# Kernel tuning notes

Measured on AMD Instinct MI355X. Metric: run time of the kernel, lower is better.

Reference implementation:

```python
import jax, jax.numpy as jnp
import numpy as np

H = 8      # heads
D = 64     # dim_head
DIM = 512  # model dim (== H*D)
LN_EPS = 1e-5


def setup_inputs() -> dict:
    key = jax.random.key(0)
    ks = jax.random.split(key, 4)
    B, N = 8, 1024
    x = jax.random.normal(ks[0], (B, N, DIM), dtype=jnp.float32)
    # params (torch Linear y = x @ W^T; we store W already transposed as (in, out))
    w_qkv = jax.random.normal(ks[1], (DIM, 3 * H * D), dtype=jnp.float32) * (DIM ** -0.5)
    w_out = jax.random.normal(ks[2], (H * D, DIM), dtype=jnp.float32) * ((H * D) ** -0.5)
    b_out = jnp.zeros((DIM,), dtype=jnp.float32)
    ln_g = jnp.ones((DIM,), dtype=jnp.float32)
    ln_b = jnp.zeros((DIM,), dtype=jnp.float32)
    return {"x": x, "w_qkv": w_qkv, "w_out": w_out, "b_out": b_out,
            "ln_g": ln_g, "ln_b": ln_b}


def reference(x, w_qkv, w_out, b_out, ln_g, ln_b):
    b, n, _ = x.shape
    qkv = x @ w_qkv                                   # [b, n, 3*H*D]
    q, k, v = jnp.split(qkv, 3, axis=-1)              # each [b, n, H*D]

    def to_heads(t):                                  # 'b n (h d) -> (b h) n d'
        return t.reshape(b, n, H, D).transpose(0, 2, 1, 3).reshape(b * H, n, D)

    q = to_heads(q)
    k = to_heads(k)
    v = to_heads(v)

    # FAITHFUL to source: k.view(b*h, -1, n) is a row-major reshape, NOT a
    # transpose, and NO scale is applied (self.scale is unused in forward).
    k_r = k.reshape(b * H, D, n)                      # [(bh), D, n] reinterpreted
    dots = jnp.matmul(q, k_r)                          # [(bh), n, n]
    attn = jax.nn.softmax(dots, axis=-1)
    out = jnp.matmul(attn, v)                          # [(bh), n, D]

    # '(b h) n d -> b n (h d)'
    out = out.reshape(b, H, n, D).transpose(0, 2, 1, 3).reshape(b, n, H * D)
    out = out @ w_out + b_out                          # to_out Linear (dropout=0)

    mu = jnp.mean(out, axis=-1, keepdims=True)
    var = jnp.var(out, axis=-1, keepdims=True)
    out = (out - mu) * jax.lax.rsqrt(var + LN_EPS) * ln_g + ln_b
    return out + x
```

## Files before the change

### kernel.cpp

```cpp
#include <hip/hip_runtime.h>

typedef unsigned short u16;
typedef unsigned int u32;
typedef __attribute__((ext_vector_type(4))) float f32x4;
typedef __attribute__((ext_vector_type(8))) short s16x8;

__device__ __forceinline__ u16 bf16_rne(float f) {
    u32 u = __float_as_uint(f);
    u32 r = u + 0x7FFFu + ((u >> 16) & 1u);
    return (u16)(r >> 16);
}

__device__ __forceinline__ u32 cvt_pk_bf16(float lo, float hi) {
    u32 r;
    asm("v_cvt_pk_bf16_f32 %0, %1, %2" : "=v"(r) : "v"(lo), "v"(hi));
    return r;
}

__device__ __forceinline__ void gl_lds16(const void* g, void* l) {
    __builtin_amdgcn_global_load_lds(
        (const __attribute__((address_space(1))) u32*)g,
        (__attribute__((address_space(3))) u32*)l, 16, 0, 0);
}

#define MFMA16(a, b, c) __builtin_amdgcn_mfma_f32_16x16x32_bf16((a), (b), (c), 0, 0, 0)

__global__ __launch_bounds__(256) void k_convert(const float* __restrict__ in,
                                                 u16* __restrict__ out, int n4) {
    int i = blockIdx.x * 256 + threadIdx.x;
    if (i >= n4) return;
    f32x4 v = *(const f32x4*)(in + (size_t)i * 4);
    u32 lo = cvt_pk_bf16(v.x, v.y);
    u32 hi = cvt_pk_bf16(v.z, v.w);
    u32* p = (u32*)(out + (size_t)i * 4);
    p[0] = lo;
    p[1] = hi;
}

__global__ __launch_bounds__(256) void k_transpose2(const float* __restrict__ w_qkv,
                                                    const float* __restrict__ w_out,
                                                    u16* __restrict__ wqkvt,
                                                    u16* __restrict__ woutt) {
    __shared__ float tile[32][33];
    const float* in;
    u16* out;
    int C, bxc;
    if (blockIdx.x < 48) { in = w_qkv; out = wqkvt; C = 1536; bxc = blockIdx.x; }
    else                 { in = w_out; out = woutt; C = 512;  bxc = blockIdx.x - 48; }
    const int R = 512;
    int bx = bxc * 32;
    int by = blockIdx.y * 32;
    int tx = threadIdx.x;
    int ty = threadIdx.y;
#pragma unroll
    for (int i = 0; i < 32; i += 8)
        tile[ty + i][tx] = in[(size_t)(by + ty + i) * C + bx + tx];
    __syncthreads();
#pragma unroll
    for (int i = 0; i < 32; i += 8)
        out[(size_t)(bx + ty + i) * R + by + tx] = bf16_rne(tile[tx][ty + i]);
}

__global__ __launch_bounds__(256) void k_qkv_gemm(
    const u16* __restrict__ xbf, const u16* __restrict__ wt,
    u16* __restrict__ qh, u16* __restrict__ kRT, u16* __restrict__ vT) {
    __shared__ __align__(16) u16 lA[2][128 * 64];
    __shared__ __align__(16) u16 lB[2][128 * 64];
    const int tid = threadIdx.x;
    const int lane = tid & 63, l15 = lane & 15, l4 = lane >> 4;
    const int wid = tid >> 6, wm = wid >> 1, wn = wid & 1;
    const int hw = blockIdx.x;
    const int e = hw & 7, idx = hw >> 3;
    const int m0 = (e + 8 * (idx / 12)) * 128;
    const int c0 = (idx % 12) * 128;

    const char* gA = (const char*)xbf + (size_t)m0 * 1024;
    const char* gB = (const char*)wt + (size_t)c0 * 1024;
    const int srow = tid >> 3;
    const int scol = (tid & 7) * 16;

    const f32x4 z4 = {0.f, 0.f, 0.f, 0.f};
    f32x4 acc[4][4];
#pragma unroll
    for (int i = 0; i < 4; ++i)
#pragma unroll
        for (int j = 0; j < 4; ++j) acc[i][j] = z4;

    auto stage = [&](int buf, int kt) {
#pragma unroll
        for (int q = 0; q < 4; ++q) {
            int row = q * 32 + srow;
            int sc = scol ^ ((row & 7) << 4);
            gl_lds16(gA + (size_t)row * 1024 + kt * 128 + sc,
                     (char*)lA[buf] + q * 4096 + tid * 16);
            gl_lds16(gB + (size_t)row * 1024 + kt * 128 + sc,
                     (char*)lB[buf] + q * 4096 + tid * 16);
        }
    };

    stage(0, 0);
    __syncthreads();
    for (int kt = 0; kt < 8; ++kt) {
        int buf = kt & 1;
        if (kt < 7) stage(buf ^ 1, kt + 1);
        s16x8 af[4][2], bfr[4][2];
#pragma unroll
        for (int i = 0; i < 4; ++i)
#pragma unroll
            for (int k2 = 0; k2 < 2; ++k2) {
                int ra = wm * 64 + i * 16 + l15;
                int ca = (k2 * 64 + l4 * 16) ^ ((ra & 7) << 4);
                af[i][k2] = *(const s16x8*)((const char*)lA[buf] + ra * 128 + ca);
                int rb = wn * 64 + i * 16 + l15;
                int cb = (k2 * 64 + l4 * 16) ^ ((rb & 7) << 4);
                bfr[i][k2] = *(const s16x8*)((const char*)lB[buf] + rb * 128 + cb);
            }
        __builtin_amdgcn_s_setprio(1);
#pragma unroll
        for (int i = 0; i < 4; ++i)
#pragma unroll
            for (int j = 0; j < 4; ++j)
#pragma unroll
                for (int k2 = 0; k2 < 2; ++k2)
                    acc[i][j] = MFMA16(af[i][k2], bfr[j][k2], acc[i][j]);
        __builtin_amdgcn_s_setprio(0);
        __syncthreads();
    }

    char* ct = (char*)lA;
    const int which = c0 >> 9;
    const int hb = (c0 & 511) >> 6;
    const int b = m0 >> 10;
    const int n0 = m0 & 1023;
    const int i4 = (m0 >> 7) & 7;

    if (which != 2) {
#pragma unroll
        for (int i = 0; i < 4; ++i)
#pragma unroll
            for (int j = 0; j < 4; ++j) {
                int col = wn * 64 + j * 16 + l15;
#pragma unroll
                for (int r = 0; r < 4; ++r) {
                    int rr = wm * 64 + i * 16 + l4 * 4 + r;
                    *(u16*)(ct + rr * 256 + ((col * 2) ^ ((rr & 7) << 4))) =
                        bf16_rne(acc[i][j][r]);
                }
            }
    } else {
#pragma unroll
        for (int i = 0; i < 4; ++i)
#pragma unroll
            for (int j = 0; j < 4; ++j) {
                int col = wn * 64 + j * 16 + l15;
#pragma unroll
                for (int r = 0; r < 4; ++r) {
                    int rr = wm * 64 + i * 16 + l4 * 4 + r;
                    *(u16*)(ct + col * 256 + ((rr * 2) ^ ((col & 7) << 4))) =
                        bf16_rne(acc[i][j][r]);
                }
            }
    }
    __syncthreads();

    if (which == 0) {
#pragma unroll
        for (int p = 0; p < 8; ++p) {
            int cid = p * 256 + tid;
            int row = cid >> 4, sub = cid & 15;
            s16x8 v = *(const s16x8*)(ct + row * 256 + ((sub * 16) ^ ((row & 7) << 4)));
            int bh = b * 8 + hb + (sub >> 3);
            *(s16x8*)((char*)qh + ((size_t)bh * 1024 + n0 + row) * 128 +
                      (sub & 7) * 16) = v;
        }
    } else if (which == 1) {
#pragma unroll
        for (int p = 0; p < 8; ++p) {
            int cid = p * 256 + tid;
            int h = cid >> 10, jb = (cid >> 6) & 15, jd = cid & 63;
            int colb = ((h * 64 + jd) * 2) ^ ((jb & 7) << 4);
            s16x8 v;
#pragma unroll
            for (int ii = 0; ii < 8; ++ii)
                v[ii] = *(const short*)(ct + (jb + ii * 16) * 256 + colb);
            int bh = b * 8 + hb + h;
            *(s16x8*)((char*)kRT + (size_t)bh * 131072 + jb * 8192 + i4 * 1024 +
                      jd * 16) = v;
        }
    } else {
#pragma unroll
        for (int p = 0; p < 8; ++p) {
            int cid = p * 256 + tid;
            int cl = cid >> 4, nc = cid & 15;
            s16x8 v = *(const s16x8*)(ct + cl * 256 + ((nc * 16) ^ ((cl & 7) << 4)));
            int bh = b * 8 + hb + (cl >> 6);
            *(s16x8*)((char*)vT + ((size_t)bh * 64 + (cl & 63)) * 2048 + n0 * 2 +
                      nc * 16) = v;
        }
    }
}

__global__ __launch_bounds__(512) void k_attn(
    const u16* __restrict__ qh, const u16* __restrict__ kRT,
    const u16* __restrict__ vT, u16* __restrict__ attn_out) {
    __shared__ __align__(16) char smem[49152];
    char* qtile = smem;
    char* ktb = smem + 16384;
    char* vtb = smem + 32768;

    const int tid = threadIdx.x;
    const int lane = tid & 63, l15 = lane & 15, l4 = lane >> 4;
    const int wid = tid >> 6;
    const int bh = blockIdx.x, mt = blockIdx.y;

    const char* kb = (const char*)kRT + (size_t)bh * 131072;
    const char* vb = (const char*)vT + (size_t)bh * 64 * 2048;
    const int srow = tid >> 3;
    const int scol = (tid & 7) * 16;

    {
        const char* gq = (const char*)qh + ((size_t)bh * 1024 + mt * 128) * 128;
#pragma unroll
        for (int q = 0; q < 2; ++q) {
            int row = q * 64 + srow;
            int sc = scol ^ ((row & 7) << 4);
            gl_lds16(gq + (size_t)row * 128 + sc, qtile + q * 8192 + tid * 16);
        }
        int i4s = (tid & 7) ^ (srow & 7);
        gl_lds16(kb + i4s * 1024 + srow * 16, ktb + tid * 16);
        int sc = scol ^ ((srow & 7) << 4);
        gl_lds16(vb + (size_t)srow * 2048 + sc, vtb + tid * 16);
    }
    __syncthreads();

    s16x8 qf[2];
#pragma unroll
    for (int k2 = 0; k2 < 2; ++k2) {
        int row = wid * 16 + l15;
        int cq = (k2 * 64 + l4 * 16) ^ ((row & 7) << 4);
        qf[k2] = *(const s16x8*)(qtile + row * 128 + cq);
    }
    __syncthreads();

    char* ptw = smem + wid * 2048;

    const f32x4 z4 = {0.f, 0.f, 0.f, 0.f};
    f32x4 o[4];
    float den = 0.f;
#pragma unroll
    for (int d4 = 0; d4 < 4; ++d4) o[d4] = z4;
    const float LOG2E = 1.4426950408889634f;

    for (int jb = 0; jb < 16; ++jb) {
        const int buf = jb & 1;
        if (jb < 15) {
            int nb = jb + 1, bufn = buf ^ 1;
            int i4s = (tid & 7) ^ (srow & 7);
            gl_lds16(kb + (size_t)nb * 8192 + i4s * 1024 + srow * 16,
                     ktb + bufn * 8192 + tid * 16);
            int sc = scol ^ ((srow & 7) << 4);
            gl_lds16(vb + (size_t)srow * 2048 + nb * 128 + sc,
                     vtb + bufn * 8192 + tid * 16);
        }
        const char* kt = ktb + buf * 8192;
        const char* vt = vtb + buf * 8192;

        s16x8 bk[4][2];
#pragma unroll
        for (int n4 = 0; n4 < 4; ++n4)
#pragma unroll
            for (int k2 = 0; k2 < 2; ++k2) {
                int rn = n4 * 16 + l15;
                int cb = (k2 * 64 + l4 * 16) ^ ((rn & 7) << 4);
                bk[n4][k2] = *(const s16x8*)(kt + rn * 128 + cb);
            }
        f32x4 s[4];
        __builtin_amdgcn_s_setprio(1);
#pragma unroll
        for (int n4 = 0; n4 < 4; ++n4) {
            s[n4] = z4;
#pragma unroll
            for (int k2 = 0; k2 < 2; ++k2)
                s[n4] = MFMA16(bk[n4][k2], qf[k2], s[n4]);
        }
        __builtin_amdgcn_s_setprio(0);

#pragma unroll
        for (int n4 = 0; n4 < 4; ++n4) {
            float e0 = exp2f(s[n4][0] * LOG2E);
            float e1 = exp2f(s[n4][1] * LOG2E);
            float e2 = exp2f(s[n4][2] * LOG2E);
            float e3 = exp2f(s[n4][3] * LOG2E);
            den += (e0 + e1) + (e2 + e3);
            uint2 w;
            w.x = cvt_pk_bf16(e0, e1);
            w.y = cvt_pk_bf16(e2, e3);
            *(uint2*)(ptw + l15 * 128 +
                      ((n4 * 32 + l4 * 8) ^ ((l15 & 7) << 4))) = w;
        }

        s16x8 bv[4][2];
#pragma unroll
        for (int d4 = 0; d4 < 4; ++d4)
#pragma unroll
            for (int k2 = 0; k2 < 2; ++k2) {
                int rn = d4 * 16 + l15;
                int cb = (k2 * 64 + l4 * 16) ^ ((rn & 7) << 4);
                bv[d4][k2] = *(const s16x8*)(vt + rn * 128 + cb);
            }

        s16x8 pa[2];
#pragma unroll
        for (int k2 = 0; k2 < 2; ++k2)
            pa[k2] = *(const s16x8*)(ptw + l15 * 128 +
                                     ((k2 * 64 + l4 * 16) ^ ((l15 & 7) << 4)));

        __builtin_amdgcn_s_setprio(1);
#pragma unroll
        for (int d4 = 0; d4 < 4; ++d4)
#pragma unroll
            for (int k2 = 0; k2 < 2; ++k2)
                o[d4] = MFMA16(bv[d4][k2], pa[k2], o[d4]);
        __builtin_amdgcn_s_setprio(0);

        if (jb < 15) __syncthreads();
    }

    den += __shfl_xor(den, 16);
    den += __shfl_xor(den, 32);
    float inv = 1.0f / den;

    {
        int row = wid * 16 + l15;
        char* ow = smem + row * 128;
#pragma unroll
        for (int d4 = 0; d4 < 4; ++d4) {
            uint2 w;
            w.x = cvt_pk_bf16(o[d4][0] * inv, o[d4][1] * inv);
            w.y = cvt_pk_bf16(o[d4][2] * inv, o[d4][3] * inv);
            *(uint2*)(ow + ((d4 * 32 + l4 * 8) ^ ((row & 7) << 4))) = w;
        }
    }
    __syncthreads();

    {
        char* dst = (char*)attn_out + ((size_t)(bh >> 3) * 1024 + mt * 128) * 1024 +
                    (bh & 7) * 128;
#pragma unroll
        for (int p = 0; p < 2; ++p) {
            int cid = p * 512 + tid;
            int row = cid >> 3, sub = cid & 7;
            s16x8 v = *(const s16x8*)(smem + row * 128 +
                                      ((sub * 16) ^ ((row & 7) << 4)));
            *(s16x8*)(dst + (size_t)row * 1024 + sub * 16) = v;
        }
    }
}

__global__ __launch_bounds__(512) void k_out_ln(
    const u16* __restrict__ aout, const u16* __restrict__ wt,
    const float* __restrict__ bias, const float* __restrict__ x,
    const float* __restrict__ g, const float* __restrict__ bb,
    float* __restrict__ out) {
    __shared__ __align__(16) char smem[131072];
    char* lB[2] = {smem, smem + 65536};
    const int tid = threadIdx.x;
    const int lane = tid & 63, l15 = lane & 15, l4 = lane >> 4;
    const int wid = tid >> 6, wm = wid >> 2, wn = wid & 3;
    const int m0 = blockIdx.x * 32;

    s16x8 af[16];
    {
        const char* arow = (const char*)aout + (size_t)(m0 + wm * 16 + l15) * 1024;
#pragma unroll
        for (int kk = 0; kk < 16; ++kk)
            af[kk] = *(const s16x8*)(arow + kk * 64 + l4 * 16);
    }

    auto stageB = [&](int buf, int kt) {
#pragma unroll
        for (int p = 0; p < 8; ++p) {
            int cid = p * 512 + tid;
            int n = cid >> 3, cc = cid & 7;
            int sc = (cc * 16) ^ ((n & 7) << 4);
            gl_lds16((const char*)wt + (size_t)n * 1024 + kt * 128 + sc,
                     lB[buf] + cid * 16);
        }
    };

    const f32x4 z4 = {0.f, 0.f, 0.f, 0.f};
    f32x4 acc[8];
#pragma unroll
    for (int j = 0; j < 8; ++j) acc[j] = z4;

    stageB(0, 0);
    __syncthreads();
    for (int kt = 0; kt < 8; ++kt) {
        int buf = kt & 1;
        if (kt < 7) stageB(buf ^ 1, kt + 1);
        s16x8 bf2[8][2];
#pragma unroll
        for (int j = 0; j < 8; ++j)
#pragma unroll
            for (int q = 0; q < 2; ++q) {
                int n = wn * 128 + j * 16 + l15;
                int cb = (q * 64 + l4 * 16) ^ ((n & 7) << 4);
                bf2[j][q] = *(const s16x8*)(lB[buf] + n * 128 + cb);
            }
        __builtin_amdgcn_s_setprio(1);
#pragma unroll
        for (int j = 0; j < 8; ++j)
#pragma unroll
            for (int q = 0; q < 2; ++q)
                acc[j] = MFMA16(af[kt * 2 + q], bf2[j][q], acc[j]);
        __builtin_amdgcn_s_setprio(0);
        __syncthreads();
    }

#pragma unroll
    for (int j = 0; j < 8; ++j) {
        int col = wn * 128 + j * 16 + l15;
        float bo = bias[col];
#pragma unroll
        for (int r = 0; r < 4; ++r) {
            int row = wm * 16 + l4 * 4 + r;
            *(float*)(smem + row * 2048 + ((col * 4) ^ ((row & 7) << 4))) =
                acc[j][r] + bo;
        }
    }
    __syncthreads();

    f32x4 g0 = *(const f32x4*)(g + lane * 8);
    f32x4 g1 = *(const f32x4*)(g + lane * 8 + 4);
    f32x4 b0 = *(const f32x4*)(bb + lane * 8);
    f32x4 b1 = *(const f32x4*)(bb + lane * 8 + 4);
#pragma unroll
    for (int rr = 0; rr < 4; ++rr) {
        int row = wid * 4 + rr;
        int sw = (row & 7) << 4;
        f32x4 v0 = *(const f32x4*)(smem + row * 2048 + ((lane * 32) ^ sw));
        f32x4 v1 = *(const f32x4*)(smem + row * 2048 + ((lane * 32 + 16) ^ sw));
        float s = v0.x + v0.y + v0.z + v0.w + v1.x + v1.y + v1.z + v1.w;
        float sq = v0.x * v0.x + v0.y * v0.y + v0.z * v0.z + v0.w * v0.w +
                   v1.x * v1.x + v1.y * v1.y + v1.z * v1.z + v1.w * v1.w;
#pragma unroll
        for (int m = 1; m < 64; m <<= 1) {
            s += __shfl_xor(s, m);
            sq += __shfl_xor(sq, m);
        }
        float mu = s * (1.0f / 512.0f);
        float var = sq * (1.0f / 512.0f) - mu * mu;
        float rstd = rsqrtf(var + 1e-5f);

        const float* xr = x + (size_t)(m0 + row) * 512 + lane * 8;
        f32x4 x0 = *(const f32x4*)(xr);
        f32x4 x1 = *(const f32x4*)(xr + 4);
        f32x4 r0, r1;
#pragma unroll
        for (int u = 0; u < 4; ++u) {
            r0[u] = (v0[u] - mu) * rstd * g0[u] + b0[u] + x0[u];
            r1[u] = (v1[u] - mu) * rstd * g1[u] + b1[u] + x1[u];
        }
        float* orow = out + (size_t)(m0 + row) * 512 + lane * 8;
        *(f32x4*)(orow) = r0;
        *(f32x4*)(orow + 4) = r1;
    }
}

extern "C" void kernel_launch(void* const* d_in, const int* in_sizes, int n_in,
                              void* d_out, int out_size, void* d_ws, size_t ws_size,
                              hipStream_t stream) {
    const float* x = (const float*)d_in[0];
    const float* w_qkv = (const float*)d_in[1];
    const float* w_out = (const float*)d_in[2];
    const float* b_out = (const float*)d_in[3];
    const float* ln_g = (const float*)d_in[4];
    const float* ln_b = (const float*)d_in[5];
    float* out = (float*)d_out;
    char* ws = (char*)d_ws;

    u16* xbf = (u16*)(ws + 0);
    u16* wqkvt = (u16*)(ws + 8388608);
    u16* woutt = (u16*)(ws + 9961472);
    u16* qh = (u16*)(ws + 10485760);
    u16* kRT = (u16*)(ws + 18874368);
    u16* vT = (u16*)(ws + 27262976);
    u16* aout = (u16*)(ws + 35651584);

    k_convert<<<4096, 256, 0, stream>>>(x, xbf, 1048576);
    k_transpose2<<<dim3(64, 16), dim3(32, 8), 0, stream>>>(w_qkv, w_out, wqkvt, woutt);
    k_qkv_gemm<<<768, 256, 0, stream>>>(xbf, wqkvt, qh, kRT, vT);
    k_attn<<<dim3(64, 8), 512, 0, stream>>>(qh, kRT, vT, aout);
    k_out_ln<<<256, 512, 0, stream>>>(aout, woutt, b_out, x, ln_g, ln_b, out);
}
```

Baseline: 81.12 us.

## Merge prep kernels and give each attention wave two query tiles

Fuses the x-to-bf16 conversion and the weight transpose kernels into one launch, removing a kernel boundary. The attention kernel goes from 8 waves of 16 query rows to 4 waves of 32 query rows each. Each K/V fragment read from LDS is then reused across two MFMA row tiles, which halves LDS fragment traffic per FLOP. The cost is more registers per wave and fewer waves per block for hiding latency.

New measurement: 85.25 us. 5.1% more time.

```diff
diff --git a/kernel.cpp b/kernel.cpp
--- a/kernel.cpp
+++ b/kernel.cpp
@@ -25,33 +25,34 @@
 
 #define MFMA16(a, b, c) __builtin_amdgcn_mfma_f32_16x16x32_bf16((a), (b), (c), 0, 0, 0)
 
-__global__ __launch_bounds__(256) void k_convert(const float* __restrict__ in,
-                                                 u16* __restrict__ out, int n4) {
-    int i = blockIdx.x * 256 + threadIdx.x;
-    if (i >= n4) return;
-    f32x4 v = *(const f32x4*)(in + (size_t)i * 4);
-    u32 lo = cvt_pk_bf16(v.x, v.y);
-    u32 hi = cvt_pk_bf16(v.z, v.w);
-    u32* p = (u32*)(out + (size_t)i * 4);
-    p[0] = lo;
-    p[1] = hi;
-}
-
-__global__ __launch_bounds__(256) void k_transpose2(const float* __restrict__ w_qkv,
-                                                    const float* __restrict__ w_out,
-                                                    u16* __restrict__ wqkvt,
-                                                    u16* __restrict__ woutt) {
+__global__ __launch_bounds__(256) void k_prep(const float* __restrict__ x,
+                                              const float* __restrict__ w_qkv,
+                                              const float* __restrict__ w_out,
+                                              u16* __restrict__ xbf,
+                                              u16* __restrict__ wqkvt,
+                                              u16* __restrict__ woutt) {
+    const int tid = threadIdx.x;
+    if (blockIdx.x < 4096) {
+        int i = blockIdx.x * 256 + tid;
+        f32x4 v = *(const f32x4*)(x + (size_t)i * 4);
+        u32* p = (u32*)(xbf + (size_t)i * 4);
+        p[0] = cvt_pk_bf16(v.x, v.y);
+        p[1] = cvt_pk_bf16(v.z, v.w);
+        return;
+    }
     __shared__ float tile[32][33];
+    int idx = blockIdx.x - 4096;
+    int bx_lin = idx & 63, by4 = idx >> 6;
     const float* in;
     u16* out;
     int C, bxc;
-    if (blockIdx.x < 48) { in = w_qkv; out = wqkvt; C = 1536; bxc = blockIdx.x; }
-    else                 { in = w_out; out = woutt; C = 512;  bxc = blockIdx.x - 48; }
+    if (bx_lin < 48) { in = w_qkv; out = wqkvt; C = 1536; bxc = bx_lin; }
+    else             { in = w_out; out = woutt; C = 512;  bxc = bx_lin - 48; }
     const int R = 512;
     int bx = bxc * 32;
-    int by = blockIdx.y * 32;
-    int tx = threadIdx.x;
-    int ty = threadIdx.y;
+    int by = by4 * 32;
+    int tx = tid & 31;
+    int ty = tid >> 5;
 #pragma unroll
     for (int i = 0; i < 32; i += 8)
         tile[ty + i][tx] = in[(size_t)(by + ty + i) * C + bx + tx];
@@ -200,7 +201,7 @@
     }
 }
 
-__global__ __launch_bounds__(512) void k_attn(
+__global__ __launch_bounds__(256) void k_attn(
     const u16* __restrict__ qh, const u16* __restrict__ kRT,
     const u16* __restrict__ vT, u16* __restrict__ attn_out) {
     __shared__ __align__(16) char smem[49152];
@@ -221,46 +222,58 @@
     {
         const char* gq = (const char*)qh + ((size_t)bh * 1024 + mt * 128) * 128;
 #pragma unroll
+        for (int q = 0; q < 4; ++q) {
+            int row = q * 32 + srow;
+            int sc = scol ^ ((row & 7) << 4);
+            gl_lds16(gq + (size_t)row * 128 + sc, qtile + q * 4096 + tid * 16);
+        }
+#pragma unroll
         for (int q = 0; q < 2; ++q) {
-            int row = q * 64 + srow;
-            int sc = scol ^ ((row & 7) << 4);
-            gl_lds16(gq + (size_t)row * 128 + sc, qtile + q * 8192 + tid * 16);
-        }
-        int i4s = (tid & 7) ^ (srow & 7);
-        gl_lds16(kb + i4s * 1024 + srow * 16, ktb + tid * 16);
-        int sc = scol ^ ((srow & 7) << 4);
-        gl_lds16(vb + (size_t)srow * 2048 + sc, vtb + tid * 16);
-    }
-    __syncthreads();
-
-    s16x8 qf[2];
-#pragma unroll
-    for (int k2 = 0; k2 < 2; ++k2) {
-        int row = wid * 16 + l15;
-        int cq = (k2 * 64 + l4 * 16) ^ ((row & 7) << 4);
-        qf[k2] = *(const s16x8*)(qtile + row * 128 + cq);
-    }
-    __syncthreads();
-
-    char* ptw = smem + wid * 2048;
+            int jd = q * 32 + srow;
+            int i4s = (tid & 7) ^ (jd & 7);
+            gl_lds16(kb + i4s * 1024 + jd * 16, ktb + q * 4096 + tid * 16);
+            int sc = scol ^ ((jd & 7) << 4);
+            gl_lds16(vb + (size_t)jd * 2048 + sc, vtb + q * 4096 + tid * 16);
+        }
+    }
+    __syncthreads();
+
+    s16x8 qf[2][2];
+#pragma unroll
+    for (int m2 = 0; m2 < 2; ++m2)
+#pragma unroll
+        for (int k2 = 0; k2 < 2; ++k2) {
+            int row = wid * 32 + m2 * 16 + l15;
+            int cq = (k2 * 64 + l4 * 16) ^ ((row & 7) << 4);
+            qf[m2][k2] = *(const s16x8*)(qtile + row * 128 + cq);
+        }
+    __syncthreads();
+
+    char* ptw = smem + wid * 4096;
 
     const f32x4 z4 = {0.f, 0.f, 0.f, 0.f};
-    f32x4 o[4];
-    float den = 0.f;
-#pragma unroll
-    for (int d4 = 0; d4 < 4; ++d4) o[d4] = z4;
+    f32x4 o[2][4];
+    float den[2] = {0.f, 0.f};
+#pragma unroll
+    for (int m2 = 0; m2 < 2; ++m2)
+#pragma unroll
+        for (int d4 = 0; d4 < 4; ++d4) o[m2][d4] = z4;
     const float LOG2E = 1.4426950408889634f;
 
     for (int jb = 0; jb < 16; ++jb) {
         const int buf = jb & 1;
         if (jb < 15) {
             int nb = jb + 1, bufn = buf ^ 1;
-            int i4s = (tid & 7) ^ (srow & 7);
-            gl_lds16(kb + (size_t)nb * 8192 + i4s * 1024 + srow * 16,
-                     ktb + bufn * 8192 + tid * 16);
-            int sc = scol ^ ((srow & 7) << 4);
-            gl_lds16(vb + (size_t)srow * 2048 + nb * 128 + sc,
-                     vtb + bufn * 8192 + tid * 16);
+#pragma unroll
+            for (int q = 0; q < 2; ++q) {
+                int jd = q * 32 + srow;
+                int i4s = (tid & 7) ^ (jd & 7);
+                gl_lds16(kb + (size_t)nb * 8192 + i4s * 1024 + jd * 16,
+                         ktb + bufn * 8192 + q * 4096 + tid * 16);
+                int sc = scol ^ ((jd & 7) << 4);
+                gl_lds16(vb + (size_t)jd * 2048 + nb * 128 + sc,
+                         vtb + bufn * 8192 + q * 4096 + tid * 16);
+            }
         }
         const char* kt = ktb + buf * 8192;
         const char* vt = vtb + buf * 8192;
@@ -274,29 +287,35 @@
                 int cb = (k2 * 64 + l4 * 16) ^ ((rn & 7) << 4);
                 bk[n4][k2] = *(const s16x8*)(kt + rn * 128 + cb);
             }
-        f32x4 s[4];
+        f32x4 s[2][4];
         __builtin_amdgcn_s_setprio(1);
 #pragma unroll
-        for (int n4 = 0; n4 < 4; ++n4) {
-            s[n4] = z4;
-#pragma unroll
-            for (int k2 = 0; k2 < 2; ++k2)
-                s[n4] = MFMA16(bk[n4][k2], qf[k2], s[n4]);
-        }
+        for (int m2 = 0; m2 < 2; ++m2)
+#pragma unroll
+            for (int n4 = 0; n4 < 4; ++n4) {
+                s[m2][n4] = z4;
+#pragma unroll
+                for (int k2 = 0; k2 < 2; ++k2)
+                    s[m2][n4] = MFMA16(bk[n4][k2], qf[m2][k2], s[m2][n4]);
+            }
         __builtin_amdgcn_s_setprio(0);
 
 #pragma unroll
-        for (int n4 = 0; n4 < 4; ++n4) {
-            float e0 = exp2f(s[n4][0] * LOG2E);
-            float e1 = exp2f(s[n4][1] * LOG2E);
-            float e2 = exp2f(s[n4][2] * LOG2E);
-            float e3 = exp2f(s[n4][3] * LOG2E);
-            den += (e0 + e1) + (e2 + e3);
-            uint2 w;
-            w.x = cvt_pk_bf16(e0, e1);
-            w.y = cvt_pk_bf16(e2, e3);
-            *(uint2*)(ptw + l15 * 128 +
-                      ((n4 * 32 + l4 * 8) ^ ((l15 & 7) << 4))) = w;
+        for (int m2 = 0; m2 < 2; ++m2) {
+            int rloc = m2 * 16 + l15;
+#pragma unroll
+            for (int n4 = 0; n4 < 4; ++n4) {
+                float e0 = exp2f(s[m2][n4][0] * LOG2E);
+                float e1 = exp2f(s[m2][n4][1] * LOG2E);
+                float e2 = exp2f(s[m2][n4][2] * LOG2E);
+                float e3 = exp2f(s[m2][n4][3] * LOG2E);
+                den[m2] += (e0 + e1) + (e2 + e3);
+                uint2 w;
+                w.x = cvt_pk_bf16(e0, e1);
+                w.y = cvt_pk_bf16(e2, e3);
+                *(uint2*)(ptw + rloc * 128 +
+                          ((n4 * 32 + l4 * 8) ^ ((rloc & 7) << 4))) = w;
+            }
         }
 
         s16x8 bv[4][2];
@@ -309,35 +328,45 @@
                 bv[d4][k2] = *(const s16x8*)(vt + rn * 128 + cb);
             }
 
-        s16x8 pa[2];
-#pragma unroll
-        for (int k2 = 0; k2 < 2; ++k2)
-            pa[k2] = *(const s16x8*)(ptw + l15 * 128 +
-                                     ((k2 * 64 + l4 * 16) ^ ((l15 & 7) << 4)));
+        s16x8 pa[2][2];
+#pragma unroll
+        for (int m2 = 0; m2 < 2; ++m2) {
+            int rloc = m2 * 16 + l15;
+#pragma unroll
+            for (int k2 = 0; k2 < 2; ++k2)
+                pa[m2][k2] = *(const s16x8*)(ptw + rloc * 128 +
+                                             ((k2 * 64 + l4 * 16) ^ ((rloc & 7) << 4)));
+        }
 
         __builtin_amdgcn_s_setprio(1);
 #pragma unroll
-        for (int d4 = 0; d4 < 4; ++d4)
-#pragma unroll
-            for (int k2 = 0; k2 < 2; ++k2)
-                o[d4] = MFMA16(bv[d4][k2], pa[k2], o[d4]);
+        for (int m2 = 0; m2 < 2; ++m2)
+#pragma unroll
+            for (int d4 = 0; d4 < 4; ++d4)
+#pragma unroll
+                for (int k2 = 0; k2 < 2; ++k2)
+                    o[m2][d4] = MFMA16(bv[d4][k2], pa[m2][k2], o[m2][d4]);
         __builtin_amdgcn_s_setprio(0);
 
         if (jb < 15) __syncthreads();
     }
 
-    den += __shfl_xor(den, 16);
-    den += __shfl_xor(den, 32);
-    float inv = 1.0f / den;
-
-    {
-        int row = wid * 16 + l15;
+#pragma unroll
+    for (int m2 = 0; m2 < 2; ++m2) {
+        den[m2] += __shfl_xor(den[m2], 16);
+        den[m2] += __shfl_xor(den[m2], 32);
+    }
+
+#pragma unroll
+    for (int m2 = 0; m2 < 2; ++m2) {
+        float inv = 1.0f / den[m2];
+        int row = wid * 32 + m2 * 16 + l15;
         char* ow = smem + row * 128;
 #pragma unroll
         for (int d4 = 0; d4 < 4; ++d4) {
             uint2 w;
-            w.x = cvt_pk_bf16(o[d4][0] * inv, o[d4][1] * inv);
-            w.y = cvt_pk_bf16(o[d4][2] * inv, o[d4][3] * inv);
+            w.x = cvt_pk_bf16(o[m2][d4][0] * inv, o[m2][d4][1] * inv);
+            w.y = cvt_pk_bf16(o[m2][d4][2] * inv, o[m2][d4][3] * inv);
             *(uint2*)(ow + ((d4 * 32 + l4 * 8) ^ ((row & 7) << 4))) = w;
         }
     }
@@ -347,8 +376,8 @@
         char* dst = (char*)attn_out + ((size_t)(bh >> 3) * 1024 + mt * 128) * 1024 +
                     (bh & 7) * 128;
 #pragma unroll
-        for (int p = 0; p < 2; ++p) {
-            int cid = p * 512 + tid;
+        for (int p = 0; p < 4; ++p) {
+            int cid = p * 256 + tid;
             int row = cid >> 3, sub = cid & 7;
             s16x8 v = *(const s16x8*)(smem + row * 128 +
                                       ((sub * 16) ^ ((row & 7) << 4)));
@@ -487,9 +516,8 @@
     u16* vT = (u16*)(ws + 27262976);
     u16* aout = (u16*)(ws + 35651584);
 
-    k_convert<<<4096, 256, 0, stream>>>(x, xbf, 1048576);
-    k_transpose2<<<dim3(64, 16), dim3(32, 8), 0, stream>>>(w_qkv, w_out, wqkvt, woutt);
+    k_prep<<<5120, 256, 0, stream>>>(x, w_qkv, w_out, xbf, wqkvt, woutt);
     k_qkv_gemm<<<768, 256, 0, stream>>>(xbf, wqkvt, qh, kRT, vT);
-    k_attn<<<dim3(64, 8), 512, 0, stream>>>(qh, kRT, vT, aout);
+    k_attn<<<dim3(64, 8), 256, 0, stream>>>(qh, kRT, vT, aout);
     k_out_ln<<<256, 512, 0, stream>>>(aout, woutt, b_out, x, ln_g, ln_b, out);
 }
```
